# Kernel optimization log

Hardware: AMD Instinct MI355X
Metric: run time of the kernel (lower is better)

Reference implementation:

```python
import jax, jax.numpy as jnp
import numpy as np

B, C_IN, H, W = 2, 32, 512, 512
HIDDEN, SIZE = 768, 16
LATENT, NUM_CLASS = 128, 21
HP, WP = H // SIZE, W // SIZE
EPS = 1e-8
TEMP = 0.5


def setup_inputs() -> dict:
    key = jax.random.key(0)
    k1, k2, k3, k4, k5 = jax.random.split(key, 5)
    x = jax.random.normal(k1, (B, C_IN, H, W), dtype=jnp.float32)
    mask = jax.random.randint(k2, (B, NUM_CLASS, HP, WP), 0, 2).astype(jnp.int32)
    conv_w = jax.random.normal(k3, (HIDDEN, C_IN, SIZE, SIZE), dtype=jnp.float32) * 0.02
    conv_b = jax.random.normal(k4, (HIDDEN,), dtype=jnp.float32) * 0.02
    latent = jax.random.normal(k5, (1, LATENT * NUM_CLASS, HIDDEN), dtype=jnp.float32)
    return {"x": x, "mask": mask, "conv_w": conv_w, "conv_b": conv_b, "latent": latent}


def reference(x, mask, conv_w, conv_b, latent):
    # Patch embedding: Conv2d(kernel=stride=16) -> (B, HIDDEN, HP, WP)
    patch = jax.lax.conv_general_dilated(
        x, conv_w, window_strides=(SIZE, SIZE), padding='VALID',
        dimension_numbers=('NCHW', 'OIHW', 'NCHW'))
    patch = patch + conv_b[None, :, None, None]
    Bv = x.shape[0]
    N = HP * WP
    patch = patch.reshape(Bv, HIDDEN, N).transpose(0, 2, 1)  # (B, N, D)
    lat = jnp.broadcast_to(latent, (Bv, LATENT * NUM_CLASS, HIDDEN))  # (B, LC, D)

    # Cosine similarity as normalized batched matmul (same math as
    # torch CosineSimilarity over broadcast (B, LC, N, D))
    dots = jnp.einsum('bld,bnd->bln', lat, patch)  # (B, LC, N)
    lat_norm = jnp.linalg.norm(lat, axis=-1)       # (B, LC)
    pat_norm = jnp.linalg.norm(patch, axis=-1)     # (B, N)
    sim = dots / jnp.maximum(lat_norm[:, :, None] * pat_norm[:, None, :], EPS)

    sim = sim.reshape(Bv, LATENT, NUM_CLASS, HP, WP).mean(axis=1)  # (B, C, HP, WP)

    m = mask.astype(jnp.float32) >= 0.5
    s = jnp.sum(jnp.where(m, jnp.exp(sim / TEMP), 0.0))
    return -jnp.log(s)
```

## Files before the change

kernel.cpp:

```cpp
#include <hip/hip_runtime.h>
#include <hip/hip_bf16.h>
#include <math.h>

#define B_     2
#define CIN    32
#define HH     512
#define WW     512
#define HID    768
#define SZ     16
#define NPATCH 1024
#define KDIM   8192
#define NCLS   21
#define LAT    128
#define LC     2688
#define NP     (B_ * NPATCH)

#define NB_CL  63
#define NB_W4  1536

typedef __attribute__((ext_vector_type(8))) short short8;
typedef __attribute__((ext_vector_type(4))) float f32x4;

__device__ __forceinline__ ushort f2bf(float f) {
    union { float f; unsigned u; } v; v.f = f;
    unsigned r = (v.u + 0x7fff + ((v.u >> 16) & 1)) >> 16;
    return (ushort)r;
}
__device__ __forceinline__ float bf2f(ushort u) {
    union { unsigned u; float f; } v; v.u = (unsigned)u << 16;
    return v.f;
}

__device__ __forceinline__ void gload16(const void* g, void* l) {
    __builtin_amdgcn_global_load_lds(
        (const __attribute__((address_space(1))) unsigned int*)g,
        (__attribute__((address_space(3))) unsigned int*)l, 16, 0, 0);
}

__device__ __forceinline__ unsigned pk2bf(float a, float b) {
    union { __hip_bfloat162 h; unsigned u; } cv;
    cv.h = __float22bfloat162_rn(make_float2(a, b));
    return cv.u;
}

__global__ __launch_bounds__(256) void k_prep(const float* __restrict__ w,
                                              const float* __restrict__ lat,
                                              ushort* __restrict__ wb,
                                              float* __restrict__ classlat) {
    const int bid = blockIdx.x;
    const int t   = threadIdx.x;

    if (bid < NB_CL) {
        const int cls  = bid / 3;
        const int dseg = bid % 3;
        const int lane = t & 63, wvv = t >> 6;
        __shared__ float sc_sh[LAT];

        for (int q = 0; q < 32; q += 2) {
            int u0 = wvv * 32 + q;
            const float* r0 = lat + (size_t)(u0 * NCLS + cls) * HID;
            const float* r1 = lat + (size_t)((u0 + 1) * NCLS + cls) * HID;
            float s0 = 0.f, s1 = 0.f;
#pragma unroll
            for (int e = 0; e < HID / 64; ++e) {
                float a = r0[lane + e * 64]; s0 += a * a;
                float b2 = r1[lane + e * 64]; s1 += b2 * b2;
            }
#pragma unroll
            for (int off = 32; off >= 1; off >>= 1) {
                s0 += __shfl_xor(s0, off, 64);
                s1 += __shfl_xor(s1, off, 64);
            }
            if (lane == 0) {
                sc_sh[u0]     = 1.0f / (128.0f * sqrtf(s0));
                sc_sh[u0 + 1] = 1.0f / (128.0f * sqrtf(s1));
            }
        }
        __syncthreads();

        const float* src = lat + (size_t)cls * HID + dseg * 256 + t;
        float a = 0.f;
        for (int u0 = 0; u0 < LAT; u0 += 8) {
            float v[8];
#pragma unroll
            for (int q = 0; q < 8; ++q)
                v[q] = src[(size_t)(u0 + q) * (NCLS * HID)];
#pragma unroll
            for (int q = 0; q < 8; ++q) a += v[q] * sc_sh[u0 + q];
        }
        classlat[cls * HID + dseg * 256 + t] = a;
    } else {
        const int cb = bid - NB_CL;
        float4 vv[4];
#pragma unroll
        for (int k = 0; k < 4; ++k)
            vv[k] = *(const float4*)(w + ((size_t)cb * 1024 + k * 256 + t) * 4);
#pragma unroll
        for (int k = 0; k < 4; ++k) {
            ushort4 o;
            o.x = f2bf(vv[k].x); o.y = f2bf(vv[k].y);
            o.z = f2bf(vv[k].z); o.w = f2bf(vv[k].w);
            *(ushort4*)(wb + ((size_t)cb * 1024 + k * 256 + t) * 4) = o;
        }
    }
}

template <int SPLITK>
__global__ __launch_bounds__(512) void k_gemm(const float* __restrict__ x,
                                              const ushort* __restrict__ wb,
                                              ushort* __restrict__ pbuf) {
    constexpr int KS = KDIM / SPLITK;
    __shared__ ushort Als[256 * 72];
    __shared__ ushort Bls[128 * 64];

    const int flat = blockIdx.x + 8 * (blockIdx.y + 6 * blockIdx.z);
    constexpr int nwg = 48 * SPLITK;
    const int wg = (flat & 7) * (nwg >> 3) + (flat >> 3);
    const int bz = wg / 48;
    const int rr = wg - bz * 48;
    const int by = rr % 6;
    const int bx = rr / 6;

    const int tid  = threadIdx.x;
    const int wv   = tid >> 6;
    const int lane = tid & 63;
    const int wm   = (wv >> 1) * 64;
    const int wn   = (wv & 1) * 64;

    const int bxb = bx >> 2;
    const int ph0 = (bx & 3) * 8;

    const size_t bbase = ((size_t)by * 128) * KDIM + (size_t)bz * KS;

    const int srow  = wv * 8 + (lane >> 3);
    const int skoff = (((lane & 7) ^ (lane >> 3)) * 8);

    f32x4 acc[4][4];
#pragma unroll
    for (int m = 0; m < 4; ++m)
#pragma unroll
        for (int n = 0; n < 4; ++n) acc[m][n] = (f32x4)(0.f);

    const int fr = lane & 15, fq = lane >> 4;
    const int frx = (fr & 7) * 8;

    for (int kk = 0; kk < KS; kk += 64) {
        const int gk = bz * KS + kk;
        const int c  = gk >> 8;
        const int i0 = (gk >> 4) & 15;
        const float* xA = x + (((size_t)(bxb * CIN + c) * HH) + ph0 * 16 + i0) * WW;

        float4 vv[8];
#pragma unroll
        for (int q = 0; q < 8; ++q) {
            int f    = q * 512 + tid;
            int row5 = f >> 7;
            int w4   = f & 127;
            vv[q] = *(const float4*)(xA + (size_t)((row5 >> 2) * 16 + (row5 & 3)) * WW
                                        + w4 * 4);
        }
#pragma unroll
        for (int q = 0; q < 2; ++q) {
            const int row = q * 64 + srow;
            gload16(&wb[bbase + (size_t)row * KDIM + kk + skoff],
                    &Bls[(q * 64 + wv * 8) * 64]);
        }
#pragma unroll
        for (int q = 0; q < 8; ++q) {
            int f    = q * 512 + tid;
            int row5 = f >> 7;
            int w4   = f & 127;
            int r    = ((row5 >> 2) << 5) + (w4 >> 2);
            int e    = ((row5 & 3) << 4) + ((w4 & 3) << 2);
            uint2 o;
            o.x = pk2bf(vv[q].x, vv[q].y);
            o.y = pk2bf(vv[q].z, vv[q].w);
            *(uint2*)&Als[r * 72 + e] = o;
        }
        __syncthreads();

#pragma unroll
        for (int s = 0; s < 2; ++s) {
            short8 af[4], bf[4];
#pragma unroll
            for (int m = 0; m < 4; ++m)
                af[m] = *(const short8*)&Als[(wm + m * 16 + fr) * 72 + s * 32 + fq * 8];
#pragma unroll
            for (int n = 0; n < 4; ++n)
                bf[n] = *(const short8*)&Bls[(wn + n * 16 + fr) * 64 + ((s * 32 + fq * 8) ^ frx)];
#pragma unroll
            for (int m = 0; m < 4; ++m)
#pragma unroll
                for (int n = 0; n < 4; ++n)
                    acc[m][n] = __builtin_amdgcn_mfma_f32_16x16x32_bf16(af[m], bf[n], acc[m][n], 0, 0, 0);
        }
        __syncthreads();
    }

#pragma unroll
    for (int m = 0; m < 4; ++m) {
#pragma unroll
        for (int n = 0; n < 4; ++n) {
            int col = by * 128 + wn + n * 16 + fr;
#pragma unroll
            for (int j = 0; j < 4; ++j) {
                int row = bx * 256 + wm + m * 16 + fq * 4 + j;
                pbuf[((size_t)row * SPLITK + bz) * HID + col] = f2bf(acc[m][n][j]);
            }
        }
    }
}

template <int SPLITK>
__global__ __launch_bounds__(256) void k_final(const ushort* __restrict__ pbuf,
                                               const float* __restrict__ conv_b,
                                               const float* __restrict__ classlat,
                                               const int* __restrict__ mask,
                                               float* __restrict__ partial) {
    const int p = blockIdx.x;
    const int b = p >> 10, n = p & 1023;
    const int t = threadIdx.x;
    const int lane = t & 63, wv = t >> 6;

    __shared__ ushort sh[SPLITK * HID];
    const ushort* pb = pbuf + (size_t)p * (SPLITK * HID);
    for (int i = t; i < SPLITK * HID / 8; i += 256)
        *(short8*)&sh[i * 8] = *(const short8*)&pb[(size_t)i * 8];
    __syncthreads();

    float f0 = conv_b[t], f1 = conv_b[t + 256], f2 = conv_b[t + 512];
#pragma unroll
    for (int z = 0; z < SPLITK; ++z) {
        f0 += bf2f(sh[z * HID + t]);
        f1 += bf2f(sh[z * HID + t + 256]);
        f2 += bf2f(sh[z * HID + t + 512]);
    }

    __shared__ float wsum[4];
    __shared__ float wdot[4][NCLS];
    __shared__ float cpart[NCLS];

    float ss = f0 * f0 + f1 * f1 + f2 * f2;
#pragma unroll
    for (int off = 32; off >= 1; off >>= 1) ss += __shfl_xor(ss, off, 64);
    if (lane == 0) wsum[wv] = ss;

    float dots[NCLS];
#pragma unroll
    for (int c = 0; c < NCLS; ++c) {
        const float* cl = classlat + c * HID;
        dots[c] = cl[t] * f0 + cl[t + 256] * f1 + cl[t + 512] * f2;
    }
#pragma unroll
    for (int c = 0; c < NCLS; ++c) {
        float v = dots[c];
#pragma unroll
        for (int off = 32; off >= 1; off >>= 1) v += __shfl_xor(v, off, 64);
        if (lane == 0) wdot[wv][c] = v;
    }
    __syncthreads();

    if (t < NCLS) {
        float tot  = wsum[0] + wsum[1] + wsum[2] + wsum[3];
        float invn = 1.0f / sqrtf(tot);
        float dot  = wdot[0][t] + wdot[1][t] + wdot[2][t] + wdot[3][t];
        float sim  = dot * invn;
        int   mv   = mask[(size_t)(b * NCLS + t) * NPATCH + n];
        cpart[t]   = (mv != 0) ? expf(sim * 2.0f) : 0.0f;
    }
    __syncthreads();
    if (t == 0) {
        float s = 0.f;
#pragma unroll
        for (int c = 0; c < NCLS; ++c) s += cpart[c];
        partial[p] = s;
    }
}

__global__ __launch_bounds__(256) void k_reduce(const float* __restrict__ partial,
                                                float* __restrict__ out) {
    int t = threadIdx.x;
    float s = 0.f;
    for (int i = t; i < NP; i += 256) s += partial[i];
#pragma unroll
    for (int off = 32; off >= 1; off >>= 1) s += __shfl_xor(s, off, 64);
    __shared__ float ws[4];
    if ((t & 63) == 0) ws[t >> 6] = s;
    __syncthreads();
    if (t == 0) out[0] = -logf(ws[0] + ws[1] + ws[2] + ws[3]);
}

extern "C" void kernel_launch(void* const* d_in, const int* in_sizes, int n_in,
                              void* d_out, int out_size, void* d_ws, size_t ws_size,
                              hipStream_t stream) {
    const float* x      = (const float*)d_in[0];
    const int*   mask   = (const int*)d_in[1];
    const float* conv_w = (const float*)d_in[2];
    const float* conv_b = (const float*)d_in[3];
    const float* latent = (const float*)d_in[4];
    float* out = (float*)d_out;

    const size_t wb_bytes   = (size_t)HID * KDIM * 2;
    const size_t pslice     = (size_t)NP * HID * 2;
    const size_t small_need = (size_t)NCLS * HID * 4 + NP * 4 + 256;

    char* base = (char*)d_ws;
    ushort* wb   = (ushort*)base;
    ushort* pbuf = (ushort*)(base + wb_bytes);

    int splitk = 1;
    const size_t fixed = wb_bytes + small_need;
    if (ws_size >= fixed + 8 * pslice)      splitk = 8;
    else if (ws_size >= fixed + 4 * pslice) splitk = 4;
    else if (ws_size >= fixed + 2 * pslice) splitk = 2;

    float* classlat = (float*)(base + wb_bytes + (size_t)splitk * pslice);
    float* partial  = classlat + NCLS * HID;

    k_prep<<<NB_CL + NB_W4, 256, 0, stream>>>(conv_w, latent, wb, classlat);

    dim3 g(NP / 256, HID / 128, splitk);
    switch (splitk) {
        case 8: k_gemm<8><<<g, 512, 0, stream>>>(x, wb, pbuf); break;
        case 4: k_gemm<4><<<g, 512, 0, stream>>>(x, wb, pbuf); break;
        case 2: k_gemm<2><<<g, 512, 0, stream>>>(x, wb, pbuf); break;
        default: k_gemm<1><<<g, 512, 0, stream>>>(x, wb, pbuf); break;
    }

    switch (splitk) {
        case 8: k_final<8><<<NP, 256, 0, stream>>>(pbuf, conv_b, classlat, mask, partial); break;
        case 4: k_final<4><<<NP, 256, 0, stream>>>(pbuf, conv_b, classlat, mask, partial); break;
        case 2: k_final<2><<<NP, 256, 0, stream>>>(pbuf, conv_b, classlat, mask, partial); break;
        default: k_final<1><<<NP, 256, 0, stream>>>(pbuf, conv_b, classlat, mask, partial); break;
    }
    k_reduce<<<1, 256, 0, stream>>>(partial, out);
}
```

Before: 103.5 us.

## Pre-convert input to bf16 and stream A tiles via direct-to-LDS loads

Adds a conversion pass in the prep kernel that writes the fp32 input image to a bf16 workspace copy. The GEMM then fetches its A (patch) tiles with global_load_lds straight into a swizzled LDS layout, instead of loading fp32 into registers, packing to bf16 and storing to padded LDS. This takes register pressure and convert/store work out of the GEMM main loop and halves the A-operand bytes it reads. The cost is an extra full read of the input plus a bf16 write in the prep kernel, and a larger workspace that may lower the chosen split-K factor.

```diff
diff --git a/kernel.cpp b/kernel.cpp
--- a/kernel.cpp
+++ b/kernel.cpp
@@ -17,6 +17,7 @@
 
 #define NB_CL  63
 #define NB_W4  1536
+#define NB_XC  4096
 
 typedef __attribute__((ext_vector_type(8))) short short8;
 typedef __attribute__((ext_vector_type(4))) float f32x4;
@@ -37,15 +38,11 @@
         (__attribute__((address_space(3))) unsigned int*)l, 16, 0, 0);
 }
 
-__device__ __forceinline__ unsigned pk2bf(float a, float b) {
-    union { __hip_bfloat162 h; unsigned u; } cv;
-    cv.h = __float22bfloat162_rn(make_float2(a, b));
-    return cv.u;
-}
-
 __global__ __launch_bounds__(256) void k_prep(const float* __restrict__ w,
+                                              const float* __restrict__ x,
                                               const float* __restrict__ lat,
                                               ushort* __restrict__ wb,
+                                              ushort* __restrict__ xbf,
                                               float* __restrict__ classlat) {
     const int bid = blockIdx.x;
     const int t   = threadIdx.x;
@@ -89,7 +86,7 @@
             for (int q = 0; q < 8; ++q) a += v[q] * sc_sh[u0 + q];
         }
         classlat[cls * HID + dseg * 256 + t] = a;
-    } else {
+    } else if (bid < NB_CL + NB_W4) {
         const int cb = bid - NB_CL;
         float4 vv[4];
 #pragma unroll
@@ -102,15 +99,29 @@
             o.z = f2bf(vv[k].z); o.w = f2bf(vv[k].w);
             *(ushort4*)(wb + ((size_t)cb * 1024 + k * 256 + t) * 4) = o;
         }
+    } else {
+        const size_t e0 = ((size_t)(bid - NB_CL - NB_W4) * 256 + t) * 16;
+        float4 vv[4];
+#pragma unroll
+        for (int k = 0; k < 4; ++k)
+            vv[k] = *(const float4*)(x + e0 + k * 4);
+        ushort o[16];
+#pragma unroll
+        for (int k = 0; k < 4; ++k) {
+            o[k * 4 + 0] = f2bf(vv[k].x); o[k * 4 + 1] = f2bf(vv[k].y);
+            o[k * 4 + 2] = f2bf(vv[k].z); o[k * 4 + 3] = f2bf(vv[k].w);
+        }
+        *(short8*)&xbf[e0]     = *(short8*)&o[0];
+        *(short8*)&xbf[e0 + 8] = *(short8*)&o[8];
     }
 }
 
 template <int SPLITK>
-__global__ __launch_bounds__(512) void k_gemm(const float* __restrict__ x,
+__global__ __launch_bounds__(512) void k_gemm(const ushort* __restrict__ xbf,
                                               const ushort* __restrict__ wb,
                                               ushort* __restrict__ pbuf) {
     constexpr int KS = KDIM / SPLITK;
-    __shared__ ushort Als[256 * 72];
+    __shared__ ushort Als[256 * 64];
     __shared__ ushort Bls[128 * 64];
 
     const int flat = blockIdx.x + 8 * (blockIdx.y + 6 * blockIdx.z);
@@ -135,6 +146,13 @@
     const int srow  = wv * 8 + (lane >> 3);
     const int skoff = (((lane & 7) ^ (lane >> 3)) * 8);
 
+    const int hi    = tid >> 8;
+    const int pw    = (tid >> 3) & 31;
+    const int esrc  = (tid & 7) ^ ((tid >> 3) & 7);
+    const size_t laneoff = (size_t)hi * 8192 + (size_t)(esrc >> 1) * 512
+                         + pw * 16 + (esrc & 1) * 8;
+    const size_t xbase0 = (size_t)bxb * 32 * 262144 + (size_t)ph0 * 8192;
+
     f32x4 acc[4][4];
 #pragma unroll
     for (int m = 0; m < 4; ++m)
@@ -148,35 +166,18 @@
         const int gk = bz * KS + kk;
         const int c  = gk >> 8;
         const int i0 = (gk >> 4) & 15;
-        const float* xA = x + (((size_t)(bxb * CIN + c) * HH) + ph0 * 16 + i0) * WW;
-
-        float4 vv[8];
-#pragma unroll
-        for (int q = 0; q < 8; ++q) {
-            int f    = q * 512 + tid;
-            int row5 = f >> 7;
-            int w4   = f & 127;
-            vv[q] = *(const float4*)(xA + (size_t)((row5 >> 2) * 16 + (row5 & 3)) * WW
-                                        + w4 * 4);
-        }
+        const ushort* xA = xbf + xbase0 + (size_t)c * 262144 + (size_t)i0 * 512
+                         + laneoff;
+
+#pragma unroll
+        for (int q = 0; q < 4; ++q)
+            gload16(xA + (size_t)q * 16384, &Als[q * 4096 + wv * 512]);
 #pragma unroll
         for (int q = 0; q < 2; ++q) {
             const int row = q * 64 + srow;
             gload16(&wb[bbase + (size_t)row * KDIM + kk + skoff],
                     &Bls[(q * 64 + wv * 8) * 64]);
         }
-#pragma unroll
-        for (int q = 0; q < 8; ++q) {
-            int f    = q * 512 + tid;
-            int row5 = f >> 7;
-            int w4   = f & 127;
-            int r    = ((row5 >> 2) << 5) + (w4 >> 2);
-            int e    = ((row5 & 3) << 4) + ((w4 & 3) << 2);
-            uint2 o;
-            o.x = pk2bf(vv[q].x, vv[q].y);
-            o.y = pk2bf(vv[q].z, vv[q].w);
-            *(uint2*)&Als[r * 72 + e] = o;
-        }
         __syncthreads();
 
 #pragma unroll
@@ -184,7 +185,7 @@
             short8 af[4], bf[4];
 #pragma unroll
             for (int m = 0; m < 4; ++m)
-                af[m] = *(const short8*)&Als[(wm + m * 16 + fr) * 72 + s * 32 + fq * 8];
+                af[m] = *(const short8*)&Als[(wm + m * 16 + fr) * 64 + ((s * 32 + fq * 8) ^ frx)];
 #pragma unroll
             for (int n = 0; n < 4; ++n)
                 bf[n] = *(const short8*)&Bls[(wn + n * 16 + fr) * 64 + ((s * 32 + fq * 8) ^ frx)];
@@ -300,31 +301,34 @@
     const float* latent = (const float*)d_in[4];
     float* out = (float*)d_out;
 
+    const size_t xbf_bytes  = (size_t)B_ * CIN * HH * WW * 2;
     const size_t wb_bytes   = (size_t)HID * KDIM * 2;
     const size_t pslice     = (size_t)NP * HID * 2;
     const size_t small_need = (size_t)NCLS * HID * 4 + NP * 4 + 256;
 
     char* base = (char*)d_ws;
-    ushort* wb   = (ushort*)base;
-    ushort* pbuf = (ushort*)(base + wb_bytes);
+    ushort* xbf  = (ushort*)base;
+    ushort* wb   = (ushort*)(base + xbf_bytes);
+    ushort* pbuf = (ushort*)(base + xbf_bytes + wb_bytes);
 
     int splitk = 1;
-    const size_t fixed = wb_bytes + small_need;
+    const size_t fixed = xbf_bytes + wb_bytes + small_need;
     if (ws_size >= fixed + 8 * pslice)      splitk = 8;
     else if (ws_size >= fixed + 4 * pslice) splitk = 4;
     else if (ws_size >= fixed + 2 * pslice) splitk = 2;
 
-    float* classlat = (float*)(base + wb_bytes + (size_t)splitk * pslice);
+    float* classlat = (float*)(base + xbf_bytes + wb_bytes + (size_t)splitk * pslice);
     float* partial  = classlat + NCLS * HID;
 
-    k_prep<<<NB_CL + NB_W4, 256, 0, stream>>>(conv_w, latent, wb, classlat);
+    k_prep<<<NB_CL + NB_W4 + NB_XC, 256, 0, stream>>>(conv_w, x, latent,
+                                                      wb, xbf, classlat);
 
     dim3 g(NP / 256, HID / 128, splitk);
     switch (splitk) {
-        case 8: k_gemm<8><<<g, 512, 0, stream>>>(x, wb, pbuf); break;
-        case 4: k_gemm<4><<<g, 512, 0, stream>>>(x, wb, pbuf); break;
-        case 2: k_gemm<2><<<g, 512, 0, stream>>>(x, wb, pbuf); break;
-        default: k_gemm<1><<<g, 512, 0, stream>>>(x, wb, pbuf); break;
+        case 8: k_gemm<8><<<g, 512, 0, stream>>>(xbf, wb, pbuf); break;
+        case 4: k_gemm<4><<<g, 512, 0, stream>>>(xbf, wb, pbuf); break;
+        case 2: k_gemm<2><<<g, 512, 0, stream>>>(xbf, wb, pbuf); break;
+        default: k_gemm<1><<<g, 512, 0, stream>>>(xbf, wb, pbuf); break;
     }
 
     switch (splitk) {
```

After: 86.55 us. 16.3% less time.

## Double-buffer GEMM tiles with direct global-to-LDS loads and in-register bf16 conversion

Applied to the files above, without the earlier changes.

Reworks the patch-embedding GEMM main loop to use double-buffered shared-memory stages with a K-step of 32. Fp32 activations are copied straight into LDS with async gload16 instead of passing through registers, and are converted to bf16 only when fragments are read. The next tile is prefetched while the current one is computed, aiming to hide global load latency and cut register staging. The cost is more LDS (fp32 A tile, two buffers), a conversion on every fragment read, more loop iterations with a sync each, and a launch-bounds occupancy hint of 4.

```diff
diff --git a/kernel.cpp b/kernel.cpp
--- a/kernel.cpp
+++ b/kernel.cpp
@@ -106,12 +106,13 @@
 }
 
 template <int SPLITK>
-__global__ __launch_bounds__(512) void k_gemm(const float* __restrict__ x,
-                                              const ushort* __restrict__ wb,
-                                              ushort* __restrict__ pbuf) {
+__global__ __launch_bounds__(512, 4) void k_gemm(const float* __restrict__ x,
+                                                 const ushort* __restrict__ wb,
+                                                 ushort* __restrict__ pbuf) {
     constexpr int KS = KDIM / SPLITK;
-    __shared__ ushort Als[256 * 72];
-    __shared__ ushort Bls[128 * 64];
+    constexpr int NT = KS / 32;
+    __shared__ float  Af[2][256 * 32];
+    __shared__ ushort Bf[2][128 * 32];
 
     const int flat = blockIdx.x + 8 * (blockIdx.y + 6 * blockIdx.z);
     constexpr int nwg = 48 * SPLITK;
@@ -130,10 +131,15 @@
     const int bxb = bx >> 2;
     const int ph0 = (bx & 3) * 8;
 
-    const size_t bbase = ((size_t)by * 128) * KDIM + (size_t)bz * KS;
-
-    const int srow  = wv * 8 + (lane >> 3);
-    const int skoff = (((lane & 7) ^ (lane >> 3)) * 8);
+    const int esrc = (tid & 7) ^ ((tid >> 3) & 7);
+    const size_t alane = (size_t)(tid >> 8) * 8192
+                       + (size_t)(esrc >> 2) * 512
+                       + (size_t)((tid >> 3) & 31) * 16
+                       + (size_t)(esrc & 3) * 4;
+    const float* xA0 = x + (size_t)bxb * 8388608 + (size_t)ph0 * 8192 + alane;
+
+    const ushort* wB0 = wb + (size_t)(by * 128 + (tid >> 2)) * KDIM
+                      + (size_t)bz * KS + (tid & 3) * 8;
 
     f32x4 acc[4][4];
 #pragma unroll
@@ -142,58 +148,52 @@
         for (int n = 0; n < 4; ++n) acc[m][n] = (f32x4)(0.f);
 
     const int fr = lane & 15, fq = lane >> 4;
-    const int frx = (fr & 7) * 8;
-
-    for (int kk = 0; kk < KS; kk += 64) {
-        const int gk = bz * KS + kk;
-        const int c  = gk >> 8;
-        const int i0 = (gk >> 4) & 15;
-        const float* xA = x + (((size_t)(bxb * CIN + c) * HH) + ph0 * 16 + i0) * WW;
-
-        float4 vv[8];
-#pragma unroll
-        for (int q = 0; q < 8; ++q) {
-            int f    = q * 512 + tid;
-            int row5 = f >> 7;
-            int w4   = f & 127;
-            vv[q] = *(const float4*)(xA + (size_t)((row5 >> 2) * 16 + (row5 & 3)) * WW
-                                        + w4 * 4);
-        }
-#pragma unroll
-        for (int q = 0; q < 2; ++q) {
-            const int row = q * 64 + srow;
-            gload16(&wb[bbase + (size_t)row * KDIM + kk + skoff],
-                    &Bls[(q * 64 + wv * 8) * 64]);
-        }
-#pragma unroll
-        for (int q = 0; q < 8; ++q) {
-            int f    = q * 512 + tid;
-            int row5 = f >> 7;
-            int w4   = f & 127;
-            int r    = ((row5 >> 2) << 5) + (w4 >> 2);
-            int e    = ((row5 & 3) << 4) + ((w4 & 3) << 2);
-            uint2 o;
-            o.x = pk2bf(vv[q].x, vv[q].y);
-            o.y = pk2bf(vv[q].z, vv[q].w);
-            *(uint2*)&Als[r * 72 + e] = o;
-        }
-        __syncthreads();
-
-#pragma unroll
-        for (int s = 0; s < 2; ++s) {
-            short8 af[4], bf[4];
-#pragma unroll
-            for (int m = 0; m < 4; ++m)
-                af[m] = *(const short8*)&Als[(wm + m * 16 + fr) * 72 + s * 32 + fq * 8];
+    const int frk = fr & 7;
+
+    auto STAGE = [&](int ks, int bsel) {
+        const int gkg = bz * KS + ks * 32;
+        const int c   = gkg >> 8;
+        const int i0  = (gkg >> 4) & 15;
+        const float* xs = xA0 + (size_t)c * 262144 + (size_t)i0 * 512;
+#pragma unroll
+        for (int q = 0; q < 4; ++q)
+            gload16(xs + (size_t)q * 16384, &Af[bsel][q * 2048 + wv * 256]);
+        gload16(wB0 + ks * 32, &Bf[bsel][tid * 8]);
+    };
+
+    auto COMPUTE = [&](int bsel) {
+        const float*  Ac = Af[bsel];
+        const ushort* Bc = Bf[bsel];
+        short8 af[4], bf[4];
+#pragma unroll
+        for (int m = 0; m < 4; ++m) {
+            const int row = (wm + m * 16 + fr) * 32;
+            const int c0  = (((2 * fq)     ^ frk) * 4);
+            const int c1  = (((2 * fq + 1) ^ frk) * 4);
+            f32x4 lo = *(const f32x4*)&Ac[row + c0];
+            f32x4 hi = *(const f32x4*)&Ac[row + c1];
+            union { unsigned u[4]; short8 s; } cv;
+            cv.u[0] = pk2bf(lo[0], lo[1]);
+            cv.u[1] = pk2bf(lo[2], lo[3]);
+            cv.u[2] = pk2bf(hi[0], hi[1]);
+            cv.u[3] = pk2bf(hi[2], hi[3]);
+            af[m] = cv.s;
+        }
+#pragma unroll
+        for (int n = 0; n < 4; ++n)
+            bf[n] = *(const short8*)&Bc[(wn + n * 16 + fr) * 32 + fq * 8];
+#pragma unroll
+        for (int m = 0; m < 4; ++m)
 #pragma unroll
             for (int n = 0; n < 4; ++n)
-                bf[n] = *(const short8*)&Bls[(wn + n * 16 + fr) * 64 + ((s * 32 + fq * 8) ^ frx)];
-#pragma unroll
-            for (int m = 0; m < 4; ++m)
-#pragma unroll
-                for (int n = 0; n < 4; ++n)
-                    acc[m][n] = __builtin_amdgcn_mfma_f32_16x16x32_bf16(af[m], bf[n], acc[m][n], 0, 0, 0);
-        }
+                acc[m][n] = __builtin_amdgcn_mfma_f32_16x16x32_bf16(af[m], bf[n], acc[m][n], 0, 0, 0);
+    };
+
+    STAGE(0, 0);
+    __syncthreads();
+    for (int ks = 0; ks < NT; ++ks) {
+        if (ks + 1 < NT) STAGE(ks + 1, (ks + 1) & 1);
+        COMPUTE(ks & 1);
         __syncthreads();
     }
 
```

Result: faster. 91.48 us (-11.6%).

## Load fp32 patches directly to LDS and convert to bf16 at fragment read

Applied to the files above, without the earlier changes.

The GEMM block tile shrinks from 256x128 with 512 threads to 128x128 with 256 threads, doubling the grid. Input patches are no longer staged through registers, converted to bf16 and stored to LDS. Instead raw fp32 data is copied global-to-LDS with direct 16-byte loads into an XOR-swizzled layout, and the bf16 conversion happens when each wave reads its A fragments. The aim is to drop the register staging and the VALU work on the load path. The cost is twice the LDS bytes per A element, repeated conversion across waves that share fragments, and more blocks that each reload B.

```diff
diff --git a/kernel.cpp b/kernel.cpp
--- a/kernel.cpp
+++ b/kernel.cpp
@@ -106,18 +106,18 @@
 }
 
 template <int SPLITK>
-__global__ __launch_bounds__(512) void k_gemm(const float* __restrict__ x,
+__global__ __launch_bounds__(256) void k_gemm(const float* __restrict__ x,
                                               const ushort* __restrict__ wb,
                                               ushort* __restrict__ pbuf) {
     constexpr int KS = KDIM / SPLITK;
-    __shared__ ushort Als[256 * 72];
+    __shared__ float  Af[128 * 64];
     __shared__ ushort Bls[128 * 64];
 
-    const int flat = blockIdx.x + 8 * (blockIdx.y + 6 * blockIdx.z);
-    constexpr int nwg = 48 * SPLITK;
+    const int flat = blockIdx.x + 16 * (blockIdx.y + 6 * blockIdx.z);
+    constexpr int nwg = 96 * SPLITK;
     const int wg = (flat & 7) * (nwg >> 3) + (flat >> 3);
-    const int bz = wg / 48;
-    const int rr = wg - bz * 48;
+    const int bz = wg / 96;
+    const int rr = wg - bz * 96;
     const int by = rr % 6;
     const int bx = rr / 6;
 
@@ -127,14 +127,20 @@
     const int wm   = (wv >> 1) * 64;
     const int wn   = (wv & 1) * 64;
 
-    const int bxb = bx >> 2;
-    const int ph0 = (bx & 3) * 8;
+    const int bxb = bx >> 3;
+    const int ph0 = (bx & 7) * 4;
 
     const size_t bbase = ((size_t)by * 128) * KDIM + (size_t)bz * KS;
 
     const int srow  = wv * 8 + (lane >> 3);
     const int skoff = (((lane & 7) ^ (lane >> 3)) * 8);
 
+    const int esrc = (tid & 15) ^ (2 * ((tid >> 4) & 7));
+    const size_t alane = (size_t)(tid >> 4) * 16
+                       + (size_t)(esrc >> 2) * 512
+                       + (size_t)(esrc & 3) * 4;
+    const float* xA0 = x + (size_t)bxb * 8388608 + (size_t)ph0 * 8192 + alane;
+
     f32x4 acc[4][4];
 #pragma unroll
     for (int m = 0; m < 4; ++m)
@@ -142,40 +148,24 @@
         for (int n = 0; n < 4; ++n) acc[m][n] = (f32x4)(0.f);
 
     const int fr = lane & 15, fq = lane >> 4;
-    const int frx = (fr & 7) * 8;
+    const int frk = fr & 7;
+    const int frx = frk * 8;
 
     for (int kk = 0; kk < KS; kk += 64) {
         const int gk = bz * KS + kk;
         const int c  = gk >> 8;
         const int i0 = (gk >> 4) & 15;
-        const float* xA = x + (((size_t)(bxb * CIN + c) * HH) + ph0 * 16 + i0) * WW;
-
-        float4 vv[8];
-#pragma unroll
-        for (int q = 0; q < 8; ++q) {
-            int f    = q * 512 + tid;
-            int row5 = f >> 7;
-            int w4   = f & 127;
-            vv[q] = *(const float4*)(xA + (size_t)((row5 >> 2) * 16 + (row5 & 3)) * WW
-                                        + w4 * 4);
-        }
-#pragma unroll
-        for (int q = 0; q < 2; ++q) {
-            const int row = q * 64 + srow;
+        const float* xs = xA0 + (size_t)c * 262144 + (size_t)i0 * 512;
+
+#pragma unroll
+        for (int q = 0; q < 8; ++q)
+            gload16(xs + (size_t)(q >> 1) * 8192 + (size_t)(q & 1) * 256,
+                    &Af[q * 1024 + wv * 256]);
+#pragma unroll
+        for (int q = 0; q < 4; ++q) {
+            const int row = q * 32 + srow;
             gload16(&wb[bbase + (size_t)row * KDIM + kk + skoff],
-                    &Bls[(q * 64 + wv * 8) * 64]);
-        }
-#pragma unroll
-        for (int q = 0; q < 8; ++q) {
-            int f    = q * 512 + tid;
-            int row5 = f >> 7;
-            int w4   = f & 127;
-            int r    = ((row5 >> 2) << 5) + (w4 >> 2);
-            int e    = ((row5 & 3) << 4) + ((w4 & 3) << 2);
-            uint2 o;
-            o.x = pk2bf(vv[q].x, vv[q].y);
-            o.y = pk2bf(vv[q].z, vv[q].w);
-            *(uint2*)&Als[r * 72 + e] = o;
+                    &Bls[q * 2048 + wv * 512]);
         }
         __syncthreads();
 
@@ -183,11 +173,22 @@
         for (int s = 0; s < 2; ++s) {
             short8 af[4], bf[4];
 #pragma unroll
-            for (int m = 0; m < 4; ++m)
-                af[m] = *(const short8*)&Als[(wm + m * 16 + fr) * 72 + s * 32 + fq * 8];
+            for (int m = 0; m < 4; ++m) {
+                const float* ap = &Af[(wm + m * 16 + fr) * 64
+                                      + 8 * ((s * 4 + fq) ^ frk)];
+                f32x4 lo = *(const f32x4*)ap;
+                f32x4 hi = *(const f32x4*)(ap + 4);
+                union { unsigned u[4]; short8 s8; } cv;
+                cv.u[0] = pk2bf(lo[0], lo[1]);
+                cv.u[1] = pk2bf(lo[2], lo[3]);
+                cv.u[2] = pk2bf(hi[0], hi[1]);
+                cv.u[3] = pk2bf(hi[2], hi[3]);
+                af[m] = cv.s8;
+            }
 #pragma unroll
             for (int n = 0; n < 4; ++n)
-                bf[n] = *(const short8*)&Bls[(wn + n * 16 + fr) * 64 + ((s * 32 + fq * 8) ^ frx)];
+                bf[n] = *(const short8*)&Bls[(wn + n * 16 + fr) * 64
+                                             + ((s * 32 + fq * 8) ^ frx)];
 #pragma unroll
             for (int m = 0; m < 4; ++m)
 #pragma unroll
@@ -204,7 +205,7 @@
             int col = by * 128 + wn + n * 16 + fr;
 #pragma unroll
             for (int j = 0; j < 4; ++j) {
-                int row = bx * 256 + wm + m * 16 + fq * 4 + j;
+                int row = bx * 128 + wm + m * 16 + fq * 4 + j;
                 pbuf[((size_t)row * SPLITK + bz) * HID + col] = f2bf(acc[m][n][j]);
             }
         }
@@ -319,12 +320,12 @@
 
     k_prep<<<NB_CL + NB_W4, 256, 0, stream>>>(conv_w, latent, wb, classlat);
 
-    dim3 g(NP / 256, HID / 128, splitk);
+    dim3 g(NP / 128, HID / 128, splitk);
     switch (splitk) {
-        case 8: k_gemm<8><<<g, 512, 0, stream>>>(x, wb, pbuf); break;
-        case 4: k_gemm<4><<<g, 512, 0, stream>>>(x, wb, pbuf); break;
-        case 2: k_gemm<2><<<g, 512, 0, stream>>>(x, wb, pbuf); break;
-        default: k_gemm<1><<<g, 512, 0, stream>>>(x, wb, pbuf); break;
+        case 8: k_gemm<8><<<g, 256, 0, stream>>>(x, wb, pbuf); break;
+        case 4: k_gemm<4><<<g, 256, 0, stream>>>(x, wb, pbuf); break;
+        case 2: k_gemm<2><<<g, 256, 0, stream>>>(x, wb, pbuf); break;
+        default: k_gemm<1><<<g, 256, 0, stream>>>(x, wb, pbuf); break;
     }
 
     switch (splitk) {
```

After: 97.22 us. 1.06x faster.
